# Kernel optimization log

Hardware: AMD Instinct MI355X
Metric: run time of the kernel (lower is better)

The kernel has to match this reference:

```python
import jax, jax.numpy as jnp
import numpy as np

ALPHA_1 = 1.0
ALPHA_2 = 1.0

def setup_inputs() -> dict:
    key = jax.random.key(0)
    k1, k2, k3, k4 = jax.random.split(key, 4)
    n, d = 4096, 1024
    # xavier_normal-ish scale for (d,d): std = sqrt(2/(d+d)) = 1/sqrt(d)
    s = 1.0 / np.sqrt(d)
    Y = jax.random.normal(k1, (n, d), dtype=jnp.float32)
    W = jax.random.normal(k2, (d, d), dtype=jnp.float32) * s
    Wf = jax.random.normal(k3, (d, d), dtype=jnp.float32) * s
    B = jax.random.normal(k4, (1, d), dtype=jnp.float32) * s
    return {"Y": Y, "W": W, "Wf": Wf, "B": B}

def reference(Y, W, Wf, B):
    # Attention: scores = Y @ (W^T W) @ Y^T = (Y W^T)(Y W^T)^T
    YWt = Y @ W.T                      # (n, d)
    A = jax.nn.softmax(YWt @ YWt.T, axis=-1)  # (n, n)
    Z = (1.0 - ALPHA_1) * Y + ALPHA_1 * (A @ Y)  # (n, d); alpha_1=1 -> A@Y
    # FFN: Wf_eff = -0.5*alpha_2*(Wf + Wf^T) + (1-alpha_2)*I; alpha_2=1
    d = Wf.shape[0]
    Wf_eff = -0.5 * ALPHA_2 * (Wf + Wf.T) + (1.0 - ALPHA_2) * jnp.eye(d, dtype=Wf.dtype)
    out = Z @ Wf_eff + B               # (n, d)
    out = jax.nn.relu(out)             # relu=True
    return out
```

## Files before the change

### kernel.cpp

```cpp
#include <hip/hip_runtime.h>
#include <cstdint>


typedef __attribute__((ext_vector_type(8))) short short8;
typedef __attribute__((ext_vector_type(4))) short short4v;
typedef __attribute__((ext_vector_type(4))) float f32x4;

__device__ __forceinline__ short f2bf(float x) {
    unsigned u = __builtin_bit_cast(unsigned, x);
    u += 0x7fffu + ((u >> 16) & 1u);
    return (short)(u >> 16);
}
__device__ __forceinline__ float bf2f(short s) {
    unsigned u = ((unsigned)(unsigned short)s) << 16;
    return __builtin_bit_cast(float, u);
}

typedef const __attribute__((address_space(1))) void* gas1_t;
typedef __attribute__((address_space(3))) void* las3_t;
__device__ __forceinline__ void cp16(const void* g, void* l) {
    __builtin_amdgcn_global_load_lds((gas1_t)(uintptr_t)g, (las3_t)(uintptr_t)l, 16, 0, 0);
}

#define MFMA16(A, B, C) __builtin_amdgcn_mfma_f32_16x16x32_bf16(A, B, C, 0, 0, 0)

__global__ __launch_bounds__(512, 1)
void gemm256_split(const short* __restrict__ Ah, const short* __restrict__ Al,
                   const short* __restrict__ Bh, const short* __restrict__ Bl,
                   short* __restrict__ Ch, short* __restrict__ Cl,
                   int M, int N, int K)
{
    __shared__ short lds[2][32768];

    const int tid  = threadIdx.x;
    const int lane = tid & 63;
    const int wave = tid >> 6;
    const int wr   = wave >> 2;
    const int wc   = wave & 3;

    const int gx  = gridDim.x;
    const int nwg = gx * gridDim.y;
    int lin = blockIdx.y * gx + blockIdx.x;
    if ((nwg & 7) == 0) { const int cpx = nwg >> 3; lin = (lin & 7) * cpx + (lin >> 3); }
    const int bm = (lin / gx) << 8;
    const int bn = (lin % gx) << 8;

    f32x4 acc[8][4];
#pragma unroll
    for (int m = 0; m < 8; ++m)
#pragma unroll
        for (int n = 0; n < 4; ++n)
#pragma unroll
            for (int q = 0; q < 4; ++q) acc[m][n][q] = 0.f;

    const int srow = tid >> 2;
    const int csw  = (tid & 3) ^ ((tid >> 3) & 3);
    const size_t oA = (size_t)(bm + srow) * K + csw * 8;
    const size_t oB = (size_t)(bn + srow) * K + csw * 8;
    const short* s0 = Ah + oA; const short* s1 = Al + oA;
    const short* s2 = Bh + oB; const short* s3 = Bl + oB;
    const size_t h128 = (size_t)128 * K;

    auto stage = [&](int t) {
        short* db = &lds[t & 1][0] + tid * 8;
        const int ko = t * 32;
        cp16(s0 + ko, db);          cp16(s0 + h128 + ko, db + 4096);
        cp16(s1 + ko, db + 8192);   cp16(s1 + h128 + ko, db + 12288);
        cp16(s2 + ko, db + 16384);  cp16(s2 + h128 + ko, db + 20480);
        cp16(s3 + ko, db + 24576);  cp16(s3 + h128 + ko, db + 28672);
    };

    const int swz  = ((lane >> 4) ^ ((lane >> 1) & 3)) * 8;
    const int aoff = (wr * 128 + (lane & 15)) * 32 + swz;
    const int boff = (wc * 64  + (lane & 15)) * 32 + swz;

    const int nt = K >> 5;
    stage(0); stage(1);

    for (int t = 0; t < nt; ++t) {
        if (t < nt - 1) { asm volatile("s_waitcnt vmcnt(8)" ::: "memory"); }
        else            { asm volatile("s_waitcnt vmcnt(0)" ::: "memory"); }
        __builtin_amdgcn_s_barrier();
        __builtin_amdgcn_sched_barrier(0);

        const short* base = &lds[t & 1][0];
        short8 fbh[4], fbl[4], fah[4], fal[4];
#pragma unroll
        for (int n = 0; n < 4; ++n) {
            fbh[n] = *(const short8*)(base + 16384 + boff + n * 512);
            fbl[n] = *(const short8*)(base + 24576 + boff + n * 512);
        }
#pragma unroll
        for (int m = 0; m < 4; ++m) {
            fah[m] = *(const short8*)(base + aoff + m * 512);
            fal[m] = *(const short8*)(base + 8192 + aoff + m * 512);
        }
        __builtin_amdgcn_s_setprio(1);
#pragma unroll
        for (int m = 0; m < 4; ++m)
#pragma unroll
            for (int n = 0; n < 4; ++n) {
                acc[m][n] = MFMA16(fah[m], fbh[n], acc[m][n]);
                acc[m][n] = MFMA16(fah[m], fbl[n], acc[m][n]);
                acc[m][n] = MFMA16(fal[m], fbh[n], acc[m][n]);
            }
        __builtin_amdgcn_s_setprio(0);
#pragma unroll
        for (int m = 0; m < 4; ++m) {
            fah[m] = *(const short8*)(base + aoff + (m + 4) * 512);
            fal[m] = *(const short8*)(base + 8192 + aoff + (m + 4) * 512);
        }
        asm volatile("s_waitcnt lgkmcnt(0)" ::: "memory");
        __builtin_amdgcn_sched_barrier(0);
        __builtin_amdgcn_s_barrier();
        __builtin_amdgcn_sched_barrier(0);
        if (t + 2 < nt) stage(t + 2);
        __builtin_amdgcn_s_setprio(1);
#pragma unroll
        for (int m = 0; m < 4; ++m)
#pragma unroll
            for (int n = 0; n < 4; ++n) {
                acc[m + 4][n] = MFMA16(fah[m], fbh[n], acc[m + 4][n]);
                acc[m + 4][n] = MFMA16(fah[m], fbl[n], acc[m + 4][n]);
                acc[m + 4][n] = MFMA16(fal[m], fbh[n], acc[m + 4][n]);
            }
        __builtin_amdgcn_s_setprio(0);
    }

    const int crow0 = bm + wr * 128 + ((lane >> 4) << 2);
    const int ccol0 = bn + wc * 64 + (lane & 15);
#pragma unroll
    for (int n = 0; n < 4; ++n) {
        const int c = ccol0 + n * 16;
#pragma unroll
        for (int m = 0; m < 8; ++m)
#pragma unroll
            for (int q = 0; q < 4; ++q) {
                const int r = crow0 + m * 16 + q;
                const float v = acc[m][n][q];
                const short hh = f2bf(v);
                Ch[(size_t)r * N + c] = hh;
                Cl[(size_t)r * N + c] = f2bf(v - bf2f(hh));
            }
    }
}

template<bool SPLIT, int OUTMODE>
__global__ __launch_bounds__(512, 2)
void gemm128_phase(const short* __restrict__ Ah, const short* __restrict__ Al,
                   const short* __restrict__ Bh, const short* __restrict__ Bl,
                   const float* __restrict__ bias, void* Co_, void* Cl_,
                   int M, int N, int K)
{
    constexpr int BK = SPLIT ? 32 : 64;
    __shared__ short lds[2][16384];

    const int tid  = threadIdx.x;
    const int lane = tid & 63;
    const int wave = tid >> 6;
    const int wr   = wave >> 2;
    const int wc   = wave & 3;

    const int gx  = gridDim.x;
    const int nwg = gx * gridDim.y;
    int lin = blockIdx.y * gx + blockIdx.x;
    if ((nwg & 7) == 0) { const int cpx = nwg >> 3; lin = (lin & 7) * cpx + (lin >> 3); }
    const int bm = (lin / gx) << 7;
    const int bn = (lin % gx) << 7;

    f32x4 acc[4][2];
#pragma unroll
    for (int m = 0; m < 4; ++m)
#pragma unroll
        for (int n = 0; n < 2; ++n)
#pragma unroll
            for (int q = 0; q < 4; ++q) acc[m][n][q] = 0.f;

    const short *p0, *p1, *p2, *p3;
    if constexpr (SPLIT) {
        const int row = tid >> 2;
        const int c4  = (tid & 3) ^ ((tid >> 3) & 3);
        const size_t oA = (size_t)(bm + row) * K + c4 * 8;
        const size_t oB = (size_t)(bn + row) * K + c4 * 8;
        p0 = Ah + oA; p1 = Al + oA; p2 = Bh + oB; p3 = Bl + oB;
    } else {
        const int row = tid >> 3;
        const int lch = (tid & 7) ^ ((tid >> 3) & 7);
        const size_t oA = (size_t)(bm + row) * K + lch * 8;
        const size_t oB = (size_t)(bn + row) * K + lch * 8;
        p0 = Ah + oA; p1 = p0 + (size_t)64 * K;
        p2 = Bh + oB; p3 = p2 + (size_t)64 * K;
    }

    auto stage = [&](int t) {
        short* db = &lds[t & 1][0] + tid * 8;
        const int ko = t * BK;
        cp16(p0 + ko, db);
        cp16(p1 + ko, db + 4096);
        cp16(p2 + ko, db + 8192);
        cp16(p3 + ko, db + 12288);
    };

    int aoff, boff;
    if constexpr (SPLIT) {
        const int swz = ((lane >> 4) ^ ((lane >> 1) & 3)) * 8;
        aoff = (wr * 64 + (lane & 15)) * 32 + swz;
        boff = (wc * 32 + (lane & 15)) * 32 + swz;
    } else {
        aoff = (wr * 64 + (lane & 15)) * 64;
        boff = (wc * 32 + (lane & 15)) * 64;
    }

    const int nt = K / BK;
    stage(0); stage(1);

    for (int t = 0; t < nt; ++t) {
        if (t < nt - 1) { asm volatile("s_waitcnt vmcnt(4)" ::: "memory"); }
        else            { asm volatile("s_waitcnt vmcnt(0)" ::: "memory"); }
        __builtin_amdgcn_s_barrier();
        __builtin_amdgcn_sched_barrier(0);

        const short* base = &lds[t & 1][0];
        if constexpr (SPLIT) {
            short8 fah[4], fal[4], fbh[2], fbl[2];
#pragma unroll
            for (int n = 0; n < 2; ++n) {
                fbh[n] = *(const short8*)(base + 8192  + boff + n * 512);
                fbl[n] = *(const short8*)(base + 12288 + boff + n * 512);
            }
#pragma unroll
            for (int m = 0; m < 4; ++m) {
                fah[m] = *(const short8*)(base + aoff + m * 512);
                fal[m] = *(const short8*)(base + 4096 + aoff + m * 512);
            }
            __builtin_amdgcn_s_setprio(1);
#pragma unroll
            for (int m = 0; m < 2; ++m)
#pragma unroll
                for (int n = 0; n < 2; ++n) {
                    acc[m][n] = MFMA16(fah[m], fbh[n], acc[m][n]);
                    acc[m][n] = MFMA16(fah[m], fbl[n], acc[m][n]);
                    acc[m][n] = MFMA16(fal[m], fbh[n], acc[m][n]);
                }
            __builtin_amdgcn_s_setprio(0);
            asm volatile("s_waitcnt lgkmcnt(0)" ::: "memory");
            __builtin_amdgcn_sched_barrier(0);
            __builtin_amdgcn_s_barrier();
            __builtin_amdgcn_sched_barrier(0);
            if (t + 2 < nt) stage(t + 2);
            __builtin_amdgcn_s_setprio(1);
#pragma unroll
            for (int m = 2; m < 4; ++m)
#pragma unroll
                for (int n = 0; n < 2; ++n) {
                    acc[m][n] = MFMA16(fah[m], fbh[n], acc[m][n]);
                    acc[m][n] = MFMA16(fah[m], fbl[n], acc[m][n]);
                    acc[m][n] = MFMA16(fal[m], fbh[n], acc[m][n]);
                }
            __builtin_amdgcn_s_setprio(0);
        } else {
            short8 fa[2][4], fb[2][2];
#pragma unroll
            for (int ks = 0; ks < 2; ++ks) {
                const int sw = ((ks * 4 + (lane >> 4)) ^ (lane & 7)) * 8;
#pragma unroll
                for (int m = 0; m < 4; ++m)
                    fa[ks][m] = *(const short8*)(base + aoff + sw + m * 1024);
#pragma unroll
                for (int n = 0; n < 2; ++n)
                    fb[ks][n] = *(const short8*)(base + 8192 + boff + sw + n * 1024);
            }
            __builtin_amdgcn_s_setprio(1);
#pragma unroll
            for (int m = 0; m < 4; ++m)
#pragma unroll
                for (int n = 0; n < 2; ++n)
                    acc[m][n] = MFMA16(fa[0][m], fb[0][n], acc[m][n]);
            __builtin_amdgcn_s_setprio(0);
            asm volatile("s_waitcnt lgkmcnt(0)" ::: "memory");
            __builtin_amdgcn_sched_barrier(0);
            __builtin_amdgcn_s_barrier();
            __builtin_amdgcn_sched_barrier(0);
            if (t + 2 < nt) stage(t + 2);
            __builtin_amdgcn_s_setprio(1);
#pragma unroll
            for (int m = 0; m < 4; ++m)
#pragma unroll
                for (int n = 0; n < 2; ++n)
                    acc[m][n] = MFMA16(fa[1][m], fb[1][n], acc[m][n]);
            __builtin_amdgcn_s_setprio(0);
        }
    }

    const int crow0 = bm + wr * 64 + ((lane >> 4) << 2);
    const int ccol0 = bn + wc * 32 + (lane & 15);
    if constexpr (OUTMODE == 2) {
        float* C = (float*)Co_;
#pragma unroll
        for (int n = 0; n < 2; ++n) {
            const int c = ccol0 + n * 16;
            const float bv = bias[c];
#pragma unroll
            for (int m = 0; m < 4; ++m)
#pragma unroll
                for (int q = 0; q < 4; ++q) {
                    const int r = crow0 + m * 16 + q;
                    C[(size_t)r * N + c] = fmaxf(acc[m][n][q] + bv, 0.f);
                }
        }
    } else if constexpr (OUTMODE == 1) {
        short* Ch = (short*)Co_;
#pragma unroll
        for (int n = 0; n < 2; ++n) {
            const int c = ccol0 + n * 16;
#pragma unroll
            for (int m = 0; m < 4; ++m)
#pragma unroll
                for (int q = 0; q < 4; ++q) {
                    const int r = crow0 + m * 16 + q;
                    Ch[(size_t)r * N + c] = f2bf(acc[m][n][q]);
                }
        }
    } else {
        short* Ch = (short*)Co_;
        short* Cl = (short*)Cl_;
#pragma unroll
        for (int n = 0; n < 2; ++n) {
            const int c = ccol0 + n * 16;
#pragma unroll
            for (int m = 0; m < 4; ++m)
#pragma unroll
                for (int q = 0; q < 4; ++q) {
                    const int r = crow0 + m * 16 + q;
                    const float v = acc[m][n][q];
                    const short hh = f2bf(v);
                    Ch[(size_t)r * N + c] = hh;
                    Cl[(size_t)r * N + c] = f2bf(v - bf2f(hh));
                }
        }
    }
}

__global__ __launch_bounds__(256)
void softmax_hi(short* __restrict__ Shi, const short* __restrict__ Slo)
{
    const int row = blockIdx.x;
    short8* ph = (short8*)(Shi + (size_t)row * 4096);
    const short8* pl = (const short8*)(Slo + (size_t)row * 4096);
    const int t = threadIdx.x;

    short8 h0 = ph[t], h1 = ph[t + 256];
    short8 l0 = pl[t], l1 = pl[t + 256];
    float x[16];
#pragma unroll
    for (int j = 0; j < 8; ++j) {
        x[j]     = bf2f(h0[j]) + bf2f(l0[j]);
        x[8 + j] = bf2f(h1[j]) + bf2f(l1[j]);
    }
    float mx = x[0];
#pragma unroll
    for (int j = 1; j < 16; ++j) mx = fmaxf(mx, x[j]);
#pragma unroll
    for (int off = 32; off > 0; off >>= 1) mx = fmaxf(mx, __shfl_xor(mx, off));

    __shared__ float rm[4], rs[4];
    const int wv = t >> 6, ln = t & 63;
    if (ln == 0) rm[wv] = mx;
    __syncthreads();
    mx = fmaxf(fmaxf(rm[0], rm[1]), fmaxf(rm[2], rm[3]));

    float s = 0.f;
#pragma unroll
    for (int j = 0; j < 16; ++j) { x[j] = __expf(x[j] - mx); s += x[j]; }
#pragma unroll
    for (int off = 32; off > 0; off >>= 1) s += __shfl_xor(s, off);
    if (ln == 0) rs[wv] = s;
    __syncthreads();
    s = rs[0] + rs[1] + rs[2] + rs[3];

    const float inv = 1.f / s;
    short8 o0, o1;
#pragma unroll
    for (int j = 0; j < 8; ++j) {
        o0[j] = f2bf(x[j] * inv);
        o1[j] = f2bf(x[8 + j] * inv);
    }
    ph[t] = o0; ph[t + 256] = o1;
}

__global__ __launch_bounds__(256)
void split_y(const float* __restrict__ Y, short* __restrict__ Yhi,
             short* __restrict__ Ylo, short* __restrict__ Yt)
{
    __shared__ float tb[64][65];
    const int rb = blockIdx.y * 64, cb = blockIdx.x * 64;
    const int t = threadIdx.x;
    const int r = t >> 4, c4 = (t & 15) * 4;
#pragma unroll
    for (int it = 0; it < 4; ++it) {
        const int row = rb + r + it * 16;
        const float4 v = *(const float4*)&Y[(size_t)row * 1024 + cb + c4];
        const float f[4] = {v.x, v.y, v.z, v.w};
        short4v h, l;
#pragma unroll
        for (int k = 0; k < 4; ++k) {
            const short hh = f2bf(f[k]);
            h[k] = hh;
            l[k] = f2bf(f[k] - bf2f(hh));
        }
        *(short4v*)&Yhi[(size_t)row * 1024 + cb + c4] = h;
        *(short4v*)&Ylo[(size_t)row * 1024 + cb + c4] = l;
        tb[r + it * 16][c4 + 0] = v.x; tb[r + it * 16][c4 + 1] = v.y;
        tb[r + it * 16][c4 + 2] = v.z; tb[r + it * 16][c4 + 3] = v.w;
    }
    __syncthreads();
    const int orow = t >> 2, oc0 = (t & 3) * 16;
    short8 h8[2];
#pragma unroll
    for (int g = 0; g < 2; ++g)
#pragma unroll
        for (int j = 0; j < 8; ++j)
            h8[g][j] = f2bf(tb[oc0 + g * 8 + j][orow]);
    const size_t ob = (size_t)(cb + orow) * 4096 + rb + oc0;
    *(short8*)&Yt[ob] = h8[0];
    *(short8*)&Yt[ob + 8] = h8[1];
}

__global__ __launch_bounds__(256)
void split_w(const float* __restrict__ Wm, short* __restrict__ Wh, short* __restrict__ Wl)
{
    const size_t idx = ((size_t)blockIdx.x * 256 + threadIdx.x) * 4;
    const float4 v = *(const float4*)&Wm[idx];
    const float f[4] = {v.x, v.y, v.z, v.w};
    short4v h, l;
#pragma unroll
    for (int k = 0; k < 4; ++k) {
        const short hh = f2bf(f[k]);
        h[k] = hh;
        l[k] = f2bf(f[k] - bf2f(hh));
    }
    *(short4v*)&Wh[idx] = h;
    *(short4v*)&Wl[idx] = l;
}

__global__ __launch_bounds__(256)
void symm_hi(const float* __restrict__ Wf, short* __restrict__ Fh)
{
    const int i  = blockIdx.x;
    const int j0 = threadIdx.x * 4;
    const float4 rv = *(const float4*)&Wf[(size_t)i * 1024 + j0];
    const float c0 = Wf[(size_t)(j0 + 0) * 1024 + i];
    const float c1 = Wf[(size_t)(j0 + 1) * 1024 + i];
    const float c2 = Wf[(size_t)(j0 + 2) * 1024 + i];
    const float c3 = Wf[(size_t)(j0 + 3) * 1024 + i];
    short4v h;
    h[0] = f2bf(-0.5f * (rv.x + c0));
    h[1] = f2bf(-0.5f * (rv.y + c1));
    h[2] = f2bf(-0.5f * (rv.z + c2));
    h[3] = f2bf(-0.5f * (rv.w + c3));
    *(short4v*)&Fh[(size_t)i * 1024 + j0] = h;
}

extern "C" void kernel_launch(void* const* d_in, const int* in_sizes, int n_in,
                              void* d_out, int out_size, void* d_ws, size_t ws_size,
                              hipStream_t stream)
{
    const float* Y  = (const float*)d_in[0];
    const float* W  = (const float*)d_in[1];
    const float* Wf = (const float*)d_in[2];
    const float* Bb = (const float*)d_in[3];
    float* out = (float*)d_out;

    const int n = 4096, d = 1024;

    char* w = (char*)d_ws;
    short* Ythi = (short*)w; w += (size_t)d * n * 2;
    short* Wfeh = (short*)w; w += (size_t)d * d * 2;
    short* YWth = (short*)w; w += (size_t)n * d * 2;
    short* YWtl = (short*)w; w += (size_t)n * d * 2;
    short* Shi  = (short*)w; w += (size_t)n * n * 2;
    short* Slo  = (short*)w; w += (size_t)n * n * 2;
    short* Yhi = Shi;
    short* Ylo = Yhi + (size_t)n * d;
    short* Whi = Ylo + (size_t)n * d;
    short* Wlo = Whi + (size_t)d * d;
    short* Zhi = YWth;

    split_y<<<dim3(16, 64), 256, 0, stream>>>(Y, Yhi, Ylo, Ythi);
    split_w<<<dim3(1024), 256, 0, stream>>>(W, Whi, Wlo);
    symm_hi<<<dim3(1024), 256, 0, stream>>>(Wf, Wfeh);

    gemm128_phase<true, 0><<<dim3(8, 32), 512, 0, stream>>>(
        Yhi, Ylo, Whi, Wlo, nullptr, YWth, YWtl, n, d, d);

    gemm256_split<<<dim3(16, 16), 512, 0, stream>>>(
        YWth, YWtl, YWth, YWtl, Shi, Slo, n, n, d);

    softmax_hi<<<dim3(n), 256, 0, stream>>>(Shi, Slo);

    gemm128_phase<false, 1><<<dim3(8, 32), 512, 0, stream>>>(
        Shi, nullptr, Ythi, nullptr, nullptr, Zhi, nullptr, n, d, n);

    gemm128_phase<false, 2><<<dim3(8, 32), 512, 0, stream>>>(
        Zhi, nullptr, Wfeh, nullptr, Bb, out, nullptr, n, d, d);
}
```

Measured before the change: 282.6 us.

## Simplify GEMM mainloop to single-stage prefetch with one barrier per tile

```diff
diff --git a/kernel.cpp b/kernel.cpp
--- a/kernel.cpp
+++ b/kernel.cpp
@@ -75,55 +75,34 @@
     const int boff = (wc * 64  + (lane & 15)) * 32 + swz;
 
     const int nt = K >> 5;
-    stage(0); stage(1);
+    stage(0);
 
     for (int t = 0; t < nt; ++t) {
-        if (t < nt - 1) { asm volatile("s_waitcnt vmcnt(8)" ::: "memory"); }
-        else            { asm volatile("s_waitcnt vmcnt(0)" ::: "memory"); }
+        asm volatile("s_waitcnt vmcnt(0)" ::: "memory");
         __builtin_amdgcn_s_barrier();
         __builtin_amdgcn_sched_barrier(0);
 
+        if (t + 1 < nt) stage(t + 1);
+
         const short* base = &lds[t & 1][0];
-        short8 fbh[4], fbl[4], fah[4], fal[4];
+        short8 fbh[4], fbl[4];
 #pragma unroll
         for (int n = 0; n < 4; ++n) {
             fbh[n] = *(const short8*)(base + 16384 + boff + n * 512);
             fbl[n] = *(const short8*)(base + 24576 + boff + n * 512);
         }
-#pragma unroll
-        for (int m = 0; m < 4; ++m) {
-            fah[m] = *(const short8*)(base + aoff + m * 512);
-            fal[m] = *(const short8*)(base + 8192 + aoff + m * 512);
-        }
         __builtin_amdgcn_s_setprio(1);
 #pragma unroll
-        for (int m = 0; m < 4; ++m)
+        for (int m = 0; m < 8; ++m) {
+            const short8 fah = *(const short8*)(base + aoff + m * 512);
+            const short8 fal = *(const short8*)(base + 8192 + aoff + m * 512);
 #pragma unroll
             for (int n = 0; n < 4; ++n) {
-                acc[m][n] = MFMA16(fah[m], fbh[n], acc[m][n]);
-                acc[m][n] = MFMA16(fah[m], fbl[n], acc[m][n]);
-                acc[m][n] = MFMA16(fal[m], fbh[n], acc[m][n]);
+                acc[m][n] = MFMA16(fah, fbh[n], acc[m][n]);
+                acc[m][n] = MFMA16(fah, fbl[n], acc[m][n]);
+                acc[m][n] = MFMA16(fal, fbh[n], acc[m][n]);
             }
-        __builtin_amdgcn_s_setprio(0);
-#pragma unroll
-        for (int m = 0; m < 4; ++m) {
-            fah[m] = *(const short8*)(base + aoff + (m + 4) * 512);
-            fal[m] = *(const short8*)(base + 8192 + aoff + (m + 4) * 512);
-        }
-        asm volatile("s_waitcnt lgkmcnt(0)" ::: "memory");
-        __builtin_amdgcn_sched_barrier(0);
-        __builtin_amdgcn_s_barrier();
-        __builtin_amdgcn_sched_barrier(0);
-        if (t + 2 < nt) stage(t + 2);
-        __builtin_amdgcn_s_setprio(1);
-#pragma unroll
-        for (int m = 0; m < 4; ++m)
-#pragma unroll
-            for (int n = 0; n < 4; ++n) {
-                acc[m + 4][n] = MFMA16(fah[m], fbh[n], acc[m + 4][n]);
-                acc[m + 4][n] = MFMA16(fah[m], fbl[n], acc[m + 4][n]);
-                acc[m + 4][n] = MFMA16(fal[m], fbh[n], acc[m + 4][n]);
-            }
+        }
         __builtin_amdgcn_s_setprio(0);
     }
 
```

New measurement: 289.5 us. 1.02x slower.
